# Kernel optimization log

Measured on AMD Instinct MI355X. Metric: run time of the kernel, lower is better.

## Reference

```python
import jax, jax.numpy as jnp
import numpy as np

D_MODEL = 1024
N_HEADS = 16
D_K = D_MODEL // N_HEADS
SCALE = float(np.sqrt(D_K))


def depthwise3(x, w, b):
    # x: [B, S, D]; w: [D, 3] (PyTorch Conv1d weight [D,1,3] squeezed); b: [D]
    # cross-correlation with kernel_size=3, padding=1, groups=D
    xp = jnp.pad(x, ((0, 0), (1, 1), (0, 0)))
    return xp[:, :-2] * w[:, 0] + xp[:, 1:-1] * w[:, 1] + xp[:, 2:] * w[:, 2] + b


def setup_inputs() -> dict:
    key = jax.random.key(0)
    ks = jax.random.split(key, 16)
    B, S, D = 2, 2048, D_MODEL
    s_lin = 1.0 / np.sqrt(D)
    s_dw = 1.0 / np.sqrt(3)
    inp = {
        "x": jax.random.normal(ks[0], (B, S, D), dtype=jnp.float32),
        "dwq_w": jax.random.uniform(ks[1], (D, 3), jnp.float32, -s_dw, s_dw),
        "dwq_b": jax.random.uniform(ks[2], (D,), jnp.float32, -s_dw, s_dw),
        "dwk_w": jax.random.uniform(ks[3], (D, 3), jnp.float32, -s_dw, s_dw),
        "dwk_b": jax.random.uniform(ks[4], (D,), jnp.float32, -s_dw, s_dw),
        "dwv_w": jax.random.uniform(ks[5], (D, 3), jnp.float32, -s_dw, s_dw),
        "dwv_b": jax.random.uniform(ks[6], (D,), jnp.float32, -s_dw, s_dw),
        "wq": jax.random.uniform(ks[7], (D, D), jnp.float32, -s_lin, s_lin),
        "bq": jax.random.uniform(ks[8], (D,), jnp.float32, -s_lin, s_lin),
        "wk": jax.random.uniform(ks[9], (D, D), jnp.float32, -s_lin, s_lin),
        "bk": jax.random.uniform(ks[10], (D,), jnp.float32, -s_lin, s_lin),
        "wv": jax.random.uniform(ks[11], (D, D), jnp.float32, -s_lin, s_lin),
        "bv": jax.random.uniform(ks[12], (D,), jnp.float32, -s_lin, s_lin),
        "wo": jax.random.uniform(ks[13], (D, D), jnp.float32, -s_lin, s_lin),
        "bo": jax.random.uniform(ks[14], (D,), jnp.float32, -s_lin, s_lin),
    }
    return inp


def reference(x, dwq_w, dwq_b, dwk_w, dwk_b, dwv_w, dwv_b,
              wq, bq, wk, bk, wv, bv, wo, bo):
    B, S, D = x.shape
    # depthwise conv (k=3, pad=1) then linear projection (PyTorch: y = x @ W^T + b)
    q = depthwise3(x, dwq_w, dwq_b) @ wq.T + bq
    k = depthwise3(x, dwk_w, dwk_b) @ wk.T + bk
    v = depthwise3(x, dwv_w, dwv_b) @ wv.T + bv
    # [B, H, S, d_k]
    q = q.reshape(B, S, N_HEADS, D_K).transpose(0, 2, 1, 3)
    k = k.reshape(B, S, N_HEADS, D_K).transpose(0, 2, 1, 3)
    v = v.reshape(B, S, N_HEADS, D_K).transpose(0, 2, 1, 3)
    scores = jnp.einsum("bhqd,bhkd->bhqk", q, k) / SCALE
    attn = jax.nn.softmax(scores, axis=-1)  # dropout=0 (eval)
    out = jnp.einsum("bhqk,bhkd->bhqd", attn, v)
    out = out.transpose(0, 2, 1, 3).reshape(B, S, D)
    return out @ wo.T + bo
```

## Files before the change

### kernel.cpp

```cpp
#include <hip/hip_runtime.h>

typedef __bf16 bf16x8 __attribute__((ext_vector_type(8)));
typedef float f32x4 __attribute__((ext_vector_type(4)));
typedef float f32x16 __attribute__((ext_vector_type(16)));
typedef unsigned short u16x8 __attribute__((ext_vector_type(8)));
typedef unsigned short u16x4 __attribute__((ext_vector_type(4)));
typedef unsigned int u32x2 __attribute__((ext_vector_type(2)));

__device__ __forceinline__ unsigned short f2bf(float f) {
  union { float f; unsigned int u; } v; v.f = f;
  unsigned int r = v.u + 0x7FFFu + ((v.u >> 16) & 1u);
  return (unsigned short)(r >> 16);
}

__device__ __forceinline__ void gload_lds16(const void* g, void* l) {
  __builtin_amdgcn_global_load_lds(
      (const __attribute__((address_space(1))) void*)g,
      (__attribute__((address_space(3))) void*)l, 16, 0, 0);
}

__global__ __launch_bounds__(256)
void conv3_kernel(const float* __restrict__ x,
                  const float* __restrict__ wq, const float* __restrict__ bq,
                  const float* __restrict__ wk, const float* __restrict__ bk,
                  const float* __restrict__ wv, const float* __restrict__ bv,
                  unsigned short* __restrict__ cq, unsigned short* __restrict__ ck,
                  unsigned short* __restrict__ cv)
{
  int t = blockIdx.x;
  int s = t & 2047;
  int d0 = threadIdx.x * 4;
  int base = t * 1024 + d0;
  f32x4 xc = *(const f32x4*)(x + base);
  f32x4 xm = (s > 0)    ? *(const f32x4*)(x + base - 1024) : f32x4{0.f,0.f,0.f,0.f};
  f32x4 xp = (s < 2047) ? *(const f32x4*)(x + base + 1024) : f32x4{0.f,0.f,0.f,0.f};

  #pragma unroll
  for (int path = 0; path < 3; path++) {
    const float* wP = (path == 0) ? wq : ((path == 1) ? wk : wv);
    const float* bP = (path == 0) ? bq : ((path == 1) ? bk : bv);
    unsigned short* oP = (path == 0) ? cq : ((path == 1) ? ck : cv);
    f32x4 w0 = *(const f32x4*)(wP + d0*3);
    f32x4 w1 = *(const f32x4*)(wP + d0*3 + 4);
    f32x4 w2 = *(const f32x4*)(wP + d0*3 + 8);
    f32x4 b4 = *(const f32x4*)(bP + d0);
    u16x4 o;
    #pragma unroll
    for (int dd = 0; dd < 4; dd++) {
      float wa, wb, wc;
      int j0 = dd*3, j1 = dd*3+1, j2 = dd*3+2;
      wa = (j0 < 4) ? w0[j0] : ((j0 < 8) ? w1[j0-4] : w2[j0-8]);
      wb = (j1 < 4) ? w0[j1] : ((j1 < 8) ? w1[j1-4] : w2[j1-8]);
      wc = (j2 < 4) ? w0[j2] : ((j2 < 8) ? w1[j2-4] : w2[j2-8]);
      o[dd] = f2bf(xm[dd]*wa + xc[dd]*wb + xp[dd]*wc + b4[dd]);
    }
    *(u16x4*)(oP + base) = o;
  }
}

__global__ __launch_bounds__(256)
void cvt_w_kernel(const float* __restrict__ w0, const float* __restrict__ w1,
                  const float* __restrict__ w2, const float* __restrict__ w3,
                  unsigned short* __restrict__ o0, unsigned short* __restrict__ o1,
                  unsigned short* __restrict__ o2, unsigned short* __restrict__ o3)
{
  const float* src; unsigned short* dst;
  switch (blockIdx.y) {
    case 0: src = w0; dst = o0; break;
    case 1: src = w1; dst = o1; break;
    case 2: src = w2; dst = o2; break;
    default: src = w3; dst = o3; break;
  }
  int i = blockIdx.x * 1024 + threadIdx.x * 4;
  f32x4 v = *(const f32x4*)(src + i);
  u16x4 o;
  #pragma unroll
  for (int j = 0; j < 4; j++) o[j] = f2bf(v[j]);
  *(u16x4*)(dst + i) = o;
}

__global__ __launch_bounds__(256)
void gemm_qkv_kernel(const unsigned short* __restrict__ cq, const unsigned short* __restrict__ ck,
                     const unsigned short* __restrict__ cv,
                     const unsigned short* __restrict__ wqb, const unsigned short* __restrict__ wkb,
                     const unsigned short* __restrict__ wvb,
                     const float* __restrict__ bq, const float* __restrict__ bk,
                     const float* __restrict__ bv,
                     unsigned short* __restrict__ qo, unsigned short* __restrict__ ko,
                     unsigned short* __restrict__ vtb)
{
  const int K = 1024;
  __shared__ alignas(16) unsigned short lA[2 * 8192];
  __shared__ alignas(16) unsigned short lB[2 * 8192];
  int z = blockIdx.z;
  const unsigned short* A = (z == 0) ? cq : ((z == 1) ? ck : cv);
  const unsigned short* W = (z == 0) ? wqb : ((z == 1) ? wkb : wvb);
  const float* bias       = (z == 0) ? bq : ((z == 1) ? bk : bv);
  float scale             = (z == 0) ? 0.125f * 1.4426950408889634f : 1.0f;

  int bm = blockIdx.y * 128, bn = blockIdx.x * 128;
  const int tid = threadIdx.x, lane = tid & 63, w = tid >> 6;
  const int lrow = lane & 15, lgrp = lane >> 4;
  const int wm = (w >> 1) * 64, wn = (w & 1) * 64;

  f32x4 acc[4][4];
  #pragma unroll
  for (int i = 0; i < 4; i++)
    #pragma unroll
    for (int j = 0; j < 4; j++) acc[i][j] = f32x4{0.f,0.f,0.f,0.f};

  auto STAGE = [&](int buf, int k0) {
    #pragma unroll
    for (int c = 0; c < 4; c++) {
      int slot_base = c * 256 + w * 64;
      int slot = slot_base + lane;
      int row = slot >> 3;
      int kc8 = ((slot & 7) ^ (row & 7)) << 3;
      gload_lds16(A + (size_t)(bm + row) * K + k0 + kc8, lA + buf * 8192 + slot_base * 8);
      gload_lds16(W + (size_t)(bn + row) * K + k0 + kc8, lB + buf * 8192 + slot_base * 8);
    }
  };

  STAGE(0, 0);
  __syncthreads();
  int cur = 0;

  for (int k0 = 0; k0 < K; k0 += 64) {
    if (k0 + 64 < K) STAGE(cur ^ 1, k0 + 64);

    #pragma unroll
    for (int kk = 0; kk < 2; kk++) {
      bf16x8 af[4], bfr[4];
      #pragma unroll
      for (int mt = 0; mt < 4; mt++) {
        int rr = wm + mt*16 + lrow;
        af[mt] = *(const bf16x8*)(lA + cur*8192 + (rr << 6) + ((((kk<<2)+lgrp) ^ (rr & 7)) << 3));
      }
      #pragma unroll
      for (int nt = 0; nt < 4; nt++) {
        int rr = wn + nt*16 + lrow;
        bfr[nt] = *(const bf16x8*)(lB + cur*8192 + (rr << 6) + ((((kk<<2)+lgrp) ^ (rr & 7)) << 3));
      }
      #pragma unroll
      for (int mt = 0; mt < 4; mt++)
        #pragma unroll
        for (int nt = 0; nt < 4; nt++)
          acc[mt][nt] = __builtin_amdgcn_mfma_f32_16x16x32_bf16(af[mt], bfr[nt], acc[mt][nt], 0, 0, 0);
    }
    __syncthreads();
    cur ^= 1;
  }

  if (z == 2) {
    #pragma unroll
    for (int mt = 0; mt < 4; mt++) {
      #pragma unroll
      for (int nt = 0; nt < 4; nt++) {
        int gn = bn + wn + nt*16 + lrow;
        float bb = bias[gn];
        int h = gn >> 6, dk = gn & 63;
        int gm0 = bm + wm + mt*16 + lgrp*4;
        int b = gm0 >> 11, s0 = gm0 & 2047;
        u16x4 pk;
        #pragma unroll
        for (int i = 0; i < 4; i++) pk[i] = f2bf(acc[mt][nt][i] + bb);
        unsigned short* dst = vtb +
            ((((size_t)(b*16 + h)) * 32 + (s0 >> 6)) * 64 + dk) * 64 + (s0 & 63);
        *(u16x4*)dst = pk;
      }
    }
  } else {
    unsigned short* O = (z == 0) ? qo : ko;
    #pragma unroll
    for (int mt = 0; mt < 4; mt++) {
      #pragma unroll
      for (int nt = 0; nt < 4; nt++) {
        int gn = bn + wn + nt*16 + lrow;
        float bb = bias[gn];
        int h = gn >> 6, dk = gn & 63;
        #pragma unroll
        for (int i = 0; i < 4; i++) {
          int gm = bm + wm + mt*16 + lgrp*4 + i;
          int b = gm >> 11, s = gm & 2047;
          float val = (acc[mt][nt][i] + bb) * scale;
          O[((size_t)(b*16 + h) * 2048 + s) * 64 + dk] = f2bf(val);
        }
      }
    }
  }
}

__global__ __launch_bounds__(256)
void gemm_out_kernel(const unsigned short* __restrict__ A, const unsigned short* __restrict__ W,
                     const float* __restrict__ bias, float* __restrict__ Out)
{
  const int K = 1024;
  __shared__ alignas(16) unsigned short lA[2 * 4096];
  __shared__ alignas(16) unsigned short lB[2 * 8192];
  int bm = blockIdx.y * 64, bn = blockIdx.x * 128;
  const int tid = threadIdx.x, lane = tid & 63, w = tid >> 6;
  const int lrow = lane & 15, lgrp = lane >> 4;
  const int wm = (w >> 1) * 32, wn = (w & 1) * 64;

  f32x4 acc[2][4];
  #pragma unroll
  for (int mt = 0; mt < 2; mt++)
    #pragma unroll
    for (int nt = 0; nt < 4; nt++) acc[mt][nt] = f32x4{0.f,0.f,0.f,0.f};

  auto STAGE = [&](int buf, int k0) {
    #pragma unroll
    for (int c = 0; c < 2; c++) {
      int slot_base = c * 256 + w * 64;
      int slot = slot_base + lane;
      int row = slot >> 3;
      int kc8 = ((slot & 7) ^ (row & 7)) << 3;
      gload_lds16(A + (size_t)(bm + row) * K + k0 + kc8, lA + buf * 4096 + slot_base * 8);
    }
    #pragma unroll
    for (int c = 0; c < 4; c++) {
      int slot_base = c * 256 + w * 64;
      int slot = slot_base + lane;
      int row = slot >> 3;
      int kc8 = ((slot & 7) ^ (row & 7)) << 3;
      gload_lds16(W + (size_t)(bn + row) * K + k0 + kc8, lB + buf * 8192 + slot_base * 8);
    }
  };

  STAGE(0, 0);
  __syncthreads();
  int cur = 0;

  for (int k0 = 0; k0 < K; k0 += 64) {
    if (k0 + 64 < K) STAGE(cur ^ 1, k0 + 64);

    #pragma unroll
    for (int kk = 0; kk < 2; kk++) {
      bf16x8 af[2], bfr[4];
      #pragma unroll
      for (int mt = 0; mt < 2; mt++) {
        int rr = wm + mt*16 + lrow;
        af[mt] = *(const bf16x8*)(lA + cur*4096 + (rr << 6) + ((((kk<<2)+lgrp) ^ (rr & 7)) << 3));
      }
      #pragma unroll
      for (int nt = 0; nt < 4; nt++) {
        int rr = wn + nt*16 + lrow;
        bfr[nt] = *(const bf16x8*)(lB + cur*8192 + (rr << 6) + ((((kk<<2)+lgrp) ^ (rr & 7)) << 3));
      }
      #pragma unroll
      for (int mt = 0; mt < 2; mt++)
        #pragma unroll
        for (int nt = 0; nt < 4; nt++)
          acc[mt][nt] = __builtin_amdgcn_mfma_f32_16x16x32_bf16(af[mt], bfr[nt], acc[mt][nt], 0, 0, 0);
    }
    __syncthreads();
    cur ^= 1;
  }

  #pragma unroll
  for (int mt = 0; mt < 2; mt++) {
    #pragma unroll
    for (int nt = 0; nt < 4; nt++) {
      int gn = bn + wn + nt*16 + lrow;
      float bb = bias[gn];
      #pragma unroll
      for (int i = 0; i < 4; i++) {
        int gm = bm + wm + mt*16 + lgrp*4 + i;
        Out[(size_t)gm * 1024 + gn] = acc[mt][nt][i] + bb;
      }
    }
  }
}

__global__ __launch_bounds__(256, 2)
void attn_kernel(const unsigned short* __restrict__ Q, const unsigned short* __restrict__ K,
                 const unsigned short* __restrict__ Vtb, unsigned short* __restrict__ O)
{
  const int S = 2048, NT = 32;
  int n = blockIdx.x;
  int xcd = n & 7, r = n >> 3;
  int bh = (xcd << 2) | (r & 3);
  int qbase = (r >> 2) * 128;

  const int tid = threadIdx.x, lane = tid & 63, w = tid >> 6;
  const int lq = lane & 31;
  const int lh = lane >> 5;
  const unsigned short* Qh = Q   + (size_t)bh * S * 64;
  const unsigned short* Kh = K   + (size_t)bh * S * 64;
  const unsigned short* Vh = Vtb + (size_t)bh * 32 * 4096;

  __shared__ alignas(16) unsigned short Kb[3][4096];
  __shared__ alignas(16) unsigned short Vb[3][4096];

  bf16x8 qf[4];
  {
    const unsigned short* qp = Qh + (size_t)(qbase + w*32 + lq) * 64 + lh * 8;
    #pragma unroll
    for (int ks = 0; ks < 4; ks++)
      qf[ks] = *(const bf16x8*)(qp + ks * 16);
  }
  bf16x8 ones;
  {
    union { __bf16 b; unsigned short u; } one; one.u = 0x3F80;
    #pragma unroll
    for (int j = 0; j < 8; j++) ones[j] = one.b;
  }

  f32x16 oacc[2], lacc;
  #pragma unroll
  for (int i = 0; i < 16; i++) { oacc[0][i] = 0.f; oacc[1][i] = 0.f; lacc[i] = 0.f; }

  auto STAGE = [&](int buf, int gt) {
    const unsigned short* gK = Kh + (size_t)gt * 4096;
    const unsigned short* gV = Vh + (size_t)gt * 4096;
    #pragma unroll
    for (int c = 0; c < 2; c++) {
      int slot_base = c * 256 + w * 64;
      int slot = slot_base + lane;
      int row = slot >> 3;
      int srcoff = (row << 6) + (((slot & 7) ^ (row & 7)) << 3);
      gload_lds16(gK + srcoff, &Kb[buf][slot_base * 8]);
      gload_lds16(gV + srcoff, &Vb[buf][slot_base * 8]);
    }
  };

  STAGE(0, 0);
  STAGE(1, 1);
  int cur = 0, stg = 2;

  for (int t = 0; t < NT; t++) {
    if (t < NT - 1) { asm volatile("s_waitcnt vmcnt(4)" ::: "memory"); }
    else            { asm volatile("s_waitcnt vmcnt(0)" ::: "memory"); }
    __builtin_amdgcn_s_barrier();
    __builtin_amdgcn_sched_barrier(0);

    if (t + 2 < NT) STAGE(stg, t + 2);

    f32x16 sacc[2];
    #pragma unroll
    for (int i = 0; i < 16; i++) { sacc[0][i] = 0.f; sacc[1][i] = 0.f; }
    #pragma unroll
    for (int ks = 0; ks < 4; ks++) {
      #pragma unroll
      for (int kt = 0; kt < 2; kt++) {
        int row = kt*32 + lq;
        bf16x8 kf = *(const bf16x8*)(&Kb[cur][(row << 6) + ((((ks<<1)+lh) ^ (row & 7)) << 3)]);
        sacc[kt] = __builtin_amdgcn_mfma_f32_32x32x16_bf16(kf, qf[ks], sacc[kt], 0, 0, 0);
      }
    }

    bf16x8 pa[4];
    #pragma unroll
    for (int kp = 0; kp < 4; kp++) {
      const int sv = kp >> 1;
      const int rb = (kp & 1) * 8;
      float p[8];
      #pragma unroll
      for (int i = 0; i < 8; i++)
        p[i] = __builtin_amdgcn_exp2f(sacc[sv][rb + i]);
      unsigned int X, Y, Z, W2;
      asm("v_cvt_pk_bf16_f32 %0, %1, %2" : "=v"(X)  : "v"(p[0]), "v"(p[1]));
      asm("v_cvt_pk_bf16_f32 %0, %1, %2" : "=v"(Y)  : "v"(p[2]), "v"(p[3]));
      asm("v_cvt_pk_bf16_f32 %0, %1, %2" : "=v"(Z)  : "v"(p[4]), "v"(p[5]));
      asm("v_cvt_pk_bf16_f32 %0, %1, %2" : "=v"(W2) : "v"(p[6]), "v"(p[7]));
      u32x2 rxz = __builtin_amdgcn_permlane32_swap(X, Z, false, false);
      u32x2 ryw = __builtin_amdgcn_permlane32_swap(Y, W2, false, false);
      union { unsigned int u[4]; bf16x8 v; } pk;
      pk.u[0] = rxz[0]; pk.u[1] = ryw[0]; pk.u[2] = rxz[1]; pk.u[3] = ryw[1];
      pa[kp] = pk.v;
    }

    __builtin_amdgcn_s_setprio(1);
    #pragma unroll
    for (int kp = 0; kp < 4; kp++) {
      #pragma unroll
      for (int dt = 0; dt < 2; dt++) {
        int row = dt*32 + lq;
        bf16x8 vf = *(const bf16x8*)(&Vb[cur][(row << 6) + ((((kp<<1)+lh) ^ (row & 7)) << 3)]);
        oacc[dt] = __builtin_amdgcn_mfma_f32_32x32x16_bf16(pa[kp], vf, oacc[dt], 0, 0, 0);
      }
      lacc = __builtin_amdgcn_mfma_f32_32x32x16_bf16(pa[kp], ones, lacc, 0, 0, 0);
    }
    __builtin_amdgcn_s_setprio(0);

    cur = (cur == 2) ? 0 : cur + 1;
    stg = (stg == 2) ? 0 : stg + 1;
  }

  int b = bh >> 4, h = bh & 15;
  #pragma unroll
  for (int reg = 0; reg < 16; reg++) {
    float rl = 1.0f / lacc[reg];
    int qrow = qbase + w*32 + (reg & 3) + 8*(reg >> 2) + 4*lh;
    unsigned short* dst = O + ((size_t)(b*2048 + qrow)) * 1024 + h*64 + lq;
    dst[0]  = f2bf(oacc[0][reg] * rl);
    dst[32] = f2bf(oacc[1][reg] * rl);
  }
}

extern "C" void kernel_launch(void* const* d_in, const int* in_sizes, int n_in,
                              void* d_out, int out_size, void* d_ws, size_t ws_size,
                              hipStream_t stream)
{
  const float* x     = (const float*)d_in[0];
  const float* dwq_w = (const float*)d_in[1];
  const float* dwq_b = (const float*)d_in[2];
  const float* dwk_w = (const float*)d_in[3];
  const float* dwk_b = (const float*)d_in[4];
  const float* dwv_w = (const float*)d_in[5];
  const float* dwv_b = (const float*)d_in[6];
  const float* wq    = (const float*)d_in[7];
  const float* bq    = (const float*)d_in[8];
  const float* wk    = (const float*)d_in[9];
  const float* bk    = (const float*)d_in[10];
  const float* wv    = (const float*)d_in[11];
  const float* bv    = (const float*)d_in[12];
  const float* wo    = (const float*)d_in[13];
  const float* bo    = (const float*)d_in[14];
  float* out = (float*)d_out;

  char* ws = (char*)d_ws;
  const size_t MB = 1024 * 1024;
  unsigned short* cq  = (unsigned short*)(ws + 0);
  unsigned short* ck  = (unsigned short*)(ws + 8*MB);
  unsigned short* cv  = (unsigned short*)(ws + 16*MB);
  unsigned short* qd  = (unsigned short*)(ws + 24*MB);
  unsigned short* kd  = (unsigned short*)(ws + 32*MB);
  unsigned short* wqb = (unsigned short*)(ws + 48*MB);
  unsigned short* wkb = (unsigned short*)(ws + 50*MB);
  unsigned short* wvb = (unsigned short*)(ws + 52*MB);
  unsigned short* wob = (unsigned short*)(ws + 54*MB);
  unsigned short* attn_out = cq;
  unsigned short* vtb      = ck;

  cvt_w_kernel<<<dim3(1024, 4), 256, 0, stream>>>(wq, wk, wv, wo, wqb, wkb, wvb, wob);
  conv3_kernel<<<4096, 256, 0, stream>>>(x, dwq_w, dwq_b, dwk_w, dwk_b, dwv_w, dwv_b, cq, ck, cv);
  gemm_qkv_kernel<<<dim3(8, 32, 3), 256, 0, stream>>>(cq, ck, cv, wqb, wkb, wvb, bq, bk, bv, qd, kd, vtb);
  attn_kernel<<<512, 256, 0, stream>>>(qd, kd, vtb, attn_out);
  gemm_out_kernel<<<dim3(8, 64), 256, 0, stream>>>(attn_out, wob, bo, out);
}
```

Measured before the change: 128.5 us.

## Triple-buffer GEMM K-loops and load V fragments directly to registers in attention

```diff
diff --git a/kernel.cpp b/kernel.cpp
--- a/kernel.cpp
+++ b/kernel.cpp
@@ -79,7 +79,7 @@
   *(u16x4*)(dst + i) = o;
 }
 
-__global__ __launch_bounds__(256)
+__global__ __launch_bounds__(256, 3)
 void gemm_qkv_kernel(const unsigned short* __restrict__ cq, const unsigned short* __restrict__ ck,
                      const unsigned short* __restrict__ cv,
                      const unsigned short* __restrict__ wqb, const unsigned short* __restrict__ wkb,
@@ -90,8 +90,8 @@
                      unsigned short* __restrict__ vtb)
 {
   const int K = 1024;
-  __shared__ alignas(16) unsigned short lA[2 * 8192];
-  __shared__ alignas(16) unsigned short lB[2 * 8192];
+  __shared__ alignas(16) unsigned short lA[3 * 4096];
+  __shared__ alignas(16) unsigned short lB[3 * 4096];
   int z = blockIdx.z;
   const unsigned short* A = (z == 0) ? cq : ((z == 1) ? ck : cv);
   const unsigned short* W = (z == 0) ? wqb : ((z == 1) ? wkb : wvb);
@@ -111,44 +111,46 @@
 
   auto STAGE = [&](int buf, int k0) {
     #pragma unroll
-    for (int c = 0; c < 4; c++) {
+    for (int c = 0; c < 2; c++) {
       int slot_base = c * 256 + w * 64;
       int slot = slot_base + lane;
-      int row = slot >> 3;
-      int kc8 = ((slot & 7) ^ (row & 7)) << 3;
-      gload_lds16(A + (size_t)(bm + row) * K + k0 + kc8, lA + buf * 8192 + slot_base * 8);
-      gload_lds16(W + (size_t)(bn + row) * K + k0 + kc8, lB + buf * 8192 + slot_base * 8);
+      int row = slot >> 2;
+      int kc8 = ((slot & 3) ^ (row & 3)) << 3;
+      gload_lds16(A + (size_t)(bm + row) * K + k0 + kc8, lA + buf * 4096 + slot_base * 8);
+      gload_lds16(W + (size_t)(bn + row) * K + k0 + kc8, lB + buf * 4096 + slot_base * 8);
     }
   };
 
   STAGE(0, 0);
-  __syncthreads();
-  int cur = 0;
-
-  for (int k0 = 0; k0 < K; k0 += 64) {
-    if (k0 + 64 < K) STAGE(cur ^ 1, k0 + 64);
-
-    #pragma unroll
-    for (int kk = 0; kk < 2; kk++) {
-      bf16x8 af[4], bfr[4];
-      #pragma unroll
-      for (int mt = 0; mt < 4; mt++) {
-        int rr = wm + mt*16 + lrow;
-        af[mt] = *(const bf16x8*)(lA + cur*8192 + (rr << 6) + ((((kk<<2)+lgrp) ^ (rr & 7)) << 3));
-      }
-      #pragma unroll
-      for (int nt = 0; nt < 4; nt++) {
-        int rr = wn + nt*16 + lrow;
-        bfr[nt] = *(const bf16x8*)(lB + cur*8192 + (rr << 6) + ((((kk<<2)+lgrp) ^ (rr & 7)) << 3));
-      }
-      #pragma unroll
-      for (int mt = 0; mt < 4; mt++)
-        #pragma unroll
-        for (int nt = 0; nt < 4; nt++)
-          acc[mt][nt] = __builtin_amdgcn_mfma_f32_16x16x32_bf16(af[mt], bfr[nt], acc[mt][nt], 0, 0, 0);
-    }
-    __syncthreads();
-    cur ^= 1;
+  STAGE(1, 32);
+  int cur = 0, stg = 2;
+
+  for (int t = 0; t < 32; t++) {
+    if (t < 31) { asm volatile("s_waitcnt vmcnt(4)" ::: "memory"); }
+    else        { asm volatile("s_waitcnt vmcnt(0)" ::: "memory"); }
+    __builtin_amdgcn_s_barrier();
+    __builtin_amdgcn_sched_barrier(0);
+    if (t + 2 < 32) STAGE(stg, (t + 2) * 32);
+
+    bf16x8 af[4], bfr[4];
+    #pragma unroll
+    for (int mt = 0; mt < 4; mt++) {
+      int rr = wm + mt*16 + lrow;
+      af[mt] = *(const bf16x8*)(lA + cur*4096 + (rr << 5) + ((lgrp ^ (rr & 3)) << 3));
+    }
+    #pragma unroll
+    for (int nt = 0; nt < 4; nt++) {
+      int rr = wn + nt*16 + lrow;
+      bfr[nt] = *(const bf16x8*)(lB + cur*4096 + (rr << 5) + ((lgrp ^ (rr & 3)) << 3));
+    }
+    #pragma unroll
+    for (int mt = 0; mt < 4; mt++)
+      #pragma unroll
+      for (int nt = 0; nt < 4; nt++)
+        acc[mt][nt] = __builtin_amdgcn_mfma_f32_16x16x32_bf16(af[mt], bfr[nt], acc[mt][nt], 0, 0, 0);
+
+    cur = (cur == 2) ? 0 : cur + 1;
+    stg = (stg == 2) ? 0 : stg + 1;
   }
 
   if (z == 2) {
@@ -161,11 +163,12 @@
         int h = gn >> 6, dk = gn & 63;
         int gm0 = bm + wm + mt*16 + lgrp*4;
         int b = gm0 >> 11, s0 = gm0 & 2047;
+        int tile = s0 >> 6, ckc = (s0 >> 3) & 7, e0 = s0 & 7;
         u16x4 pk;
         #pragma unroll
         for (int i = 0; i < 4; i++) pk[i] = f2bf(acc[mt][nt][i] + bb);
         unsigned short* dst = vtb +
-            ((((size_t)(b*16 + h)) * 32 + (s0 >> 6)) * 64 + dk) * 64 + (s0 & 63);
+            ((((size_t)(b*16 + h) * 32 + tile) * 8 + ckc) * 64 + dk) * 8 + e0;
         *(u16x4*)dst = pk;
       }
     }
@@ -195,8 +198,8 @@
                      const float* __restrict__ bias, float* __restrict__ Out)
 {
   const int K = 1024;
-  __shared__ alignas(16) unsigned short lA[2 * 4096];
-  __shared__ alignas(16) unsigned short lB[2 * 8192];
+  __shared__ alignas(16) unsigned short lA[3 * 2048];
+  __shared__ alignas(16) unsigned short lB[3 * 4096];
   int bm = blockIdx.y * 64, bn = blockIdx.x * 128;
   const int tid = threadIdx.x, lane = tid & 63, w = tid >> 6;
   const int lrow = lane & 15, lgrp = lane >> 4;
@@ -209,52 +212,52 @@
     for (int nt = 0; nt < 4; nt++) acc[mt][nt] = f32x4{0.f,0.f,0.f,0.f};
 
   auto STAGE = [&](int buf, int k0) {
+    {
+      int slot = tid;
+      int row = slot >> 2;
+      int kc8 = ((slot & 3) ^ (row & 3)) << 3;
+      gload_lds16(A + (size_t)(bm + row) * K + k0 + kc8, lA + buf * 2048 + (w * 64) * 8);
+    }
     #pragma unroll
     for (int c = 0; c < 2; c++) {
       int slot_base = c * 256 + w * 64;
       int slot = slot_base + lane;
-      int row = slot >> 3;
-      int kc8 = ((slot & 7) ^ (row & 7)) << 3;
-      gload_lds16(A + (size_t)(bm + row) * K + k0 + kc8, lA + buf * 4096 + slot_base * 8);
-    }
-    #pragma unroll
-    for (int c = 0; c < 4; c++) {
-      int slot_base = c * 256 + w * 64;
-      int slot = slot_base + lane;
-      int row = slot >> 3;
-      int kc8 = ((slot & 7) ^ (row & 7)) << 3;
-      gload_lds16(W + (size_t)(bn + row) * K + k0 + kc8, lB + buf * 8192 + slot_base * 8);
+      int row = slot >> 2;
+      int kc8 = ((slot & 3) ^ (row & 3)) << 3;
+      gload_lds16(W + (size_t)(bn + row) * K + k0 + kc8, lB + buf * 4096 + slot_base * 8);
     }
   };
 
   STAGE(0, 0);
-  __syncthreads();
-  int cur = 0;
-
-  for (int k0 = 0; k0 < K; k0 += 64) {
-    if (k0 + 64 < K) STAGE(cur ^ 1, k0 + 64);
-
-    #pragma unroll
-    for (int kk = 0; kk < 2; kk++) {
-      bf16x8 af[2], bfr[4];
-      #pragma unroll
-      for (int mt = 0; mt < 2; mt++) {
-        int rr = wm + mt*16 + lrow;
-        af[mt] = *(const bf16x8*)(lA + cur*4096 + (rr << 6) + ((((kk<<2)+lgrp) ^ (rr & 7)) << 3));
-      }
-      #pragma unroll
-      for (int nt = 0; nt < 4; nt++) {
-        int rr = wn + nt*16 + lrow;
-        bfr[nt] = *(const bf16x8*)(lB + cur*8192 + (rr << 6) + ((((kk<<2)+lgrp) ^ (rr & 7)) << 3));
-      }
-      #pragma unroll
-      for (int mt = 0; mt < 2; mt++)
-        #pragma unroll
-        for (int nt = 0; nt < 4; nt++)
-          acc[mt][nt] = __builtin_amdgcn_mfma_f32_16x16x32_bf16(af[mt], bfr[nt], acc[mt][nt], 0, 0, 0);
-    }
-    __syncthreads();
-    cur ^= 1;
+  STAGE(1, 32);
+  int cur = 0, stg = 2;
+
+  for (int t = 0; t < 32; t++) {
+    if (t < 31) { asm volatile("s_waitcnt vmcnt(3)" ::: "memory"); }
+    else        { asm volatile("s_waitcnt vmcnt(0)" ::: "memory"); }
+    __builtin_amdgcn_s_barrier();
+    __builtin_amdgcn_sched_barrier(0);
+    if (t + 2 < 32) STAGE(stg, (t + 2) * 32);
+
+    bf16x8 af[2], bfr[4];
+    #pragma unroll
+    for (int mt = 0; mt < 2; mt++) {
+      int rr = wm + mt*16 + lrow;
+      af[mt] = *(const bf16x8*)(lA + cur*2048 + (rr << 5) + ((lgrp ^ (rr & 3)) << 3));
+    }
+    #pragma unroll
+    for (int nt = 0; nt < 4; nt++) {
+      int rr = wn + nt*16 + lrow;
+      bfr[nt] = *(const bf16x8*)(lB + cur*4096 + (rr << 5) + ((lgrp ^ (rr & 3)) << 3));
+    }
+    #pragma unroll
+    for (int mt = 0; mt < 2; mt++)
+      #pragma unroll
+      for (int nt = 0; nt < 4; nt++)
+        acc[mt][nt] = __builtin_amdgcn_mfma_f32_16x16x32_bf16(af[mt], bfr[nt], acc[mt][nt], 0, 0, 0);
+
+    cur = (cur == 2) ? 0 : cur + 1;
+    stg = (stg == 2) ? 0 : stg + 1;
   }
 
   #pragma unroll
@@ -290,7 +293,6 @@
   const unsigned short* Vh = Vtb + (size_t)bh * 32 * 4096;
 
   __shared__ alignas(16) unsigned short Kb[3][4096];
-  __shared__ alignas(16) unsigned short Vb[3][4096];
 
   bf16x8 qf[4];
   {
@@ -312,7 +314,6 @@
 
   auto STAGE = [&](int buf, int gt) {
     const unsigned short* gK = Kh + (size_t)gt * 4096;
-    const unsigned short* gV = Vh + (size_t)gt * 4096;
     #pragma unroll
     for (int c = 0; c < 2; c++) {
       int slot_base = c * 256 + w * 64;
@@ -320,20 +321,29 @@
       int row = slot >> 3;
       int srcoff = (row << 6) + (((slot & 7) ^ (row & 7)) << 3);
       gload_lds16(gK + srcoff, &Kb[buf][slot_base * 8]);
-      gload_lds16(gV + srcoff, &Vb[buf][slot_base * 8]);
     }
   };
-
+  auto VLOAD = [&](bf16x8 (&dst)[8], int gt) {
+    const unsigned short* gV = Vh + (size_t)gt * 4096;
+    #pragma unroll
+    for (int kp = 0; kp < 4; kp++)
+      #pragma unroll
+      for (int dt = 0; dt < 2; dt++)
+        dst[kp*2 + dt] = *(const bf16x8*)(gV + (((kp << 1) + lh) << 9) + ((dt*32 + lq) << 3));
+  };
+
+  bf16x8 vfA[8], vfB[8];
+  VLOAD(vfA, 0);
   STAGE(0, 0);
   STAGE(1, 1);
   int cur = 0, stg = 2;
 
-  for (int t = 0; t < NT; t++) {
-    if (t < NT - 1) { asm volatile("s_waitcnt vmcnt(4)" ::: "memory"); }
+  auto body = [&](int t, bf16x8 (&vcur)[8], bf16x8 (&vnext)[8]) {
+    if (t < NT - 1) { asm volatile("s_waitcnt vmcnt(2)" ::: "memory"); }
     else            { asm volatile("s_waitcnt vmcnt(0)" ::: "memory"); }
     __builtin_amdgcn_s_barrier();
     __builtin_amdgcn_sched_barrier(0);
-
+    if (t + 1 < NT) VLOAD(vnext, t + 1);
     if (t + 2 < NT) STAGE(stg, t + 2);
 
     f32x16 sacc[2];
@@ -374,17 +384,19 @@
     #pragma unroll
     for (int kp = 0; kp < 4; kp++) {
       #pragma unroll
-      for (int dt = 0; dt < 2; dt++) {
-        int row = dt*32 + lq;
-        bf16x8 vf = *(const bf16x8*)(&Vb[cur][(row << 6) + ((((kp<<1)+lh) ^ (row & 7)) << 3)]);
-        oacc[dt] = __builtin_amdgcn_mfma_f32_32x32x16_bf16(pa[kp], vf, oacc[dt], 0, 0, 0);
-      }
+      for (int dt = 0; dt < 2; dt++)
+        oacc[dt] = __builtin_amdgcn_mfma_f32_32x32x16_bf16(pa[kp], vcur[kp*2 + dt], oacc[dt], 0, 0, 0);
       lacc = __builtin_amdgcn_mfma_f32_32x32x16_bf16(pa[kp], ones, lacc, 0, 0, 0);
     }
     __builtin_amdgcn_s_setprio(0);
 
     cur = (cur == 2) ? 0 : cur + 1;
     stg = (stg == 2) ? 0 : stg + 1;
+  };
+
+  for (int t = 0; t < NT; t += 2) {
+    body(t,     vfA, vfB);
+    body(t + 1, vfB, vfA);
   }
 
   int b = bh >> 4, h = bh & 15;
```

After: 131.4 us. +2.3%, slower.
